# Optimization experiments

Measured on AMD Instinct MI355X. Metric: run time of the kernel, lower is better.

The kernel has to match this reference:

```python
import jax, jax.numpy as jnp
import numpy as np

EPS = 1e-12  # torch F.normalize eps


def _l1_normalize(x, axis):
    denom = jnp.maximum(jnp.sum(jnp.abs(x), axis=axis, keepdims=True), EPS)
    return x / denom


def setup_inputs() -> dict:
    key = jax.random.key(0)
    k1, k2, k3, k4, k5 = jax.random.split(key, 5)
    B, N, M, F_atom, F_bond, F_out = 16, 1024, 12, 128, 32, 128
    stdv = 1.0 / np.sqrt(F_out)
    atom = jax.random.normal(k1, (B, N, F_atom), dtype=jnp.float32)
    bond = jax.random.normal(k2, (B, N, M, F_bond), dtype=jnp.float32)
    adj_matrix = jax.random.randint(k3, (B, N, M), 0, N, dtype=jnp.int64)
    weight_atom_1 = jax.random.uniform(k4, (F_atom, F_out), dtype=jnp.float32, minval=-stdv, maxval=stdv)
    bias_atom_1 = jax.random.uniform(k5, (F_out,), dtype=jnp.float32, minval=-stdv, maxval=stdv)
    return {
        "atom": atom,
        "bond": bond,
        "adj_matrix": adj_matrix,
        "weight_atom_1": weight_atom_1,
        "bias_atom_1": bias_atom_1,
    }


def reference(atom, bond, adj_matrix, weight_atom_1, bias_atom_1):
    # atom: (B,N,F); bond: (B,N,M,Fb); adj_matrix: (B,N,M)
    # Per-batch neighbor gather: atom_neighbor[b,n,m] = atom[b, adj[b,n,m]]
    atom_neighbor = jax.vmap(lambda a, idx: a[idx])(atom, adj_matrix)  # (B,N,M,F)
    atom_neighbor = jnp.mean(atom_neighbor, axis=-2)  # (B,N,F)

    # Bond-norm chain
    bond_norm = jnp.sqrt(jnp.sum(bond * bond, axis=-1))       # (B,N,M) L2 norm
    bond_norm = bond_norm ** (-2.0)                            # inverse square
    bond_norm = _l1_normalize(bond_norm, axis=-1)              # over M
    bond_norm = jnp.prod(bond_norm, axis=2)                    # (B,N)
    bond_norm = _l1_normalize(bond_norm, axis=0)               # over B
    bond_norm = bond_norm ** (-1.0)
    bond_norm = _l1_normalize(bond_norm, axis=1)               # over N

    atom_update = (atom + atom_neighbor) * bond_norm[:, :, None]
    atom_update = jnp.matmul(atom_update, weight_atom_1) + bias_atom_1
    return jax.nn.relu(atom_update)
```

## Files before the change

### kernel.cpp

```cpp
#include <hip/hip_runtime.h>
#include <hip/hip_bf16.h>

#define EPS 1e-12f

typedef __bf16 bf16x8 __attribute__((ext_vector_type(8)));
typedef float  f32x4  __attribute__((ext_vector_type(4)));


__global__ __launch_bounds__(256) void k_bond(const float* __restrict__ bond,
                                              float* __restrict__ p_out) {
    const int gwave = (blockIdx.x * 256 + threadIdx.x) >> 6;
    const int lane  = threadIdx.x & 63;
    const float* base = bond + (size_t)gwave * 384;

    float x[12];
#pragma unroll
    for (int i = 0; i < 6; ++i) {
        float v  = base[lane + 64 * i];
        float sq = v * v;
#pragma unroll
        for (int off = 16; off >= 1; off >>= 1) sq += __shfl_xor(sq, off);
        float s0 = __shfl(sq, 0);
        float s1 = __shfl(sq, 32);
        x[2 * i]     = 1.0f / s0;
        x[2 * i + 1] = 1.0f / s1;
    }
    float sum = 0.f;
#pragma unroll
    for (int m = 0; m < 12; ++m) sum += x[m];
    float d = fmaxf(sum, EPS);
    float prod = 1.f;
#pragma unroll
    for (int m = 0; m < 12; ++m) prod *= x[m] / d;
    if (lane == 0) p_out[gwave] = prod;
}

__global__ __launch_bounds__(256) void k_norm(const float* __restrict__ p,
                                              const float* __restrict__ W,
                                              float* __restrict__ scale,
                                              __bf16* __restrict__ Wt) {
    const int t = threadIdx.x;
    if (blockIdx.x < 16) {
        const int b = blockIdx.x;
        float r[4];
        float partial = 0.f;
#pragma unroll
        for (int i = 0; i < 4; ++i) {
            int n = t + 256 * i;
            float cs = 0.f;
#pragma unroll
            for (int bb = 0; bb < 16; ++bb) cs += p[bb * 1024 + n];
            float y = p[b * 1024 + n] / fmaxf(cs, EPS);
            r[i] = 1.0f / y;
            partial += r[i];
        }
        __shared__ float red[4];
        float v = partial;
#pragma unroll
        for (int off = 32; off >= 1; off >>= 1) v += __shfl_xor(v, off);
        if ((t & 63) == 0) red[t >> 6] = v;
        __syncthreads();
        float S = fmaxf(red[0] + red[1] + red[2] + red[3], EPS);
#pragma unroll
        for (int i = 0; i < 4; ++i) {
            int n = t + 256 * i;
            scale[b * 1024 + n] = r[i] / S;
        }
    } else {
        const int kb = blockIdx.x - 16;
        for (int idx = t; idx < 8 * 128; idx += 256) {
            int k = kb * 8 + (idx >> 7);
            int j = idx & 127;
            Wt[j * 128 + k] = (__bf16)W[k * 128 + j];
        }
    }
}

__global__ __launch_bounds__(256) void k_main(const float* __restrict__ atom,
                                              const int* __restrict__ adj,
                                              const float* __restrict__ scale,
                                              const __bf16* __restrict__ Wt,
                                              const float* __restrict__ bias,
                                              float* __restrict__ out) {
    __shared__ __bf16 uA[32][136];
    __shared__ float  sScale[32];
    __shared__ int    sAdj[32 * 12];

    const int t = threadIdx.x;
    const int rowbase = blockIdx.x * 32;
    const int b = rowbase >> 10;

    if (t < 32) sScale[t] = scale[rowbase + t];
    for (int idx = t; idx < 32 * 12; idx += 256) sAdj[idx] = adj[rowbase * 12 + idx];
    __syncthreads();

    {
        const int j = t & 127;
        const int half = t >> 7;
        const float* atomB = atom + (size_t)b * (1024 * 128);
#pragma unroll 4
        for (int r = half; r < 32; r += 2) {
            float accn = 0.f;
#pragma unroll
            for (int m = 0; m < 12; ++m) {
                int idx = sAdj[r * 12 + m];
                accn += atomB[idx * 128 + j];
            }
            float u = (atom[(size_t)(rowbase + r) * 128 + j] + accn * (1.0f / 12.0f)) * sScale[r];
            uA[r][j] = (__bf16)u;
        }
    }
    __syncthreads();

    const int wave = t >> 6, lane = t & 63;
    const int r0 = (wave >> 1) * 16;
    const int c0 = (wave & 1) * 64;
    const int quad = lane >> 4, lrow = lane & 15;

    bf16x8 aF[4];
#pragma unroll
    for (int kc = 0; kc < 4; ++kc)
        aF[kc] = *(const bf16x8*)&uA[r0 + lrow][kc * 32 + quad * 8];

    f32x4 acc[4];
#pragma unroll
    for (int nt = 0; nt < 4; ++nt) acc[nt] = (f32x4){0.f, 0.f, 0.f, 0.f};

#pragma unroll
    for (int nt = 0; nt < 4; ++nt) {
        const int col = c0 + nt * 16 + lrow;
        const __bf16* wb = Wt + col * 128 + quad * 8;
#pragma unroll
        for (int kc = 0; kc < 4; ++kc) {
            bf16x8 bF = *(const bf16x8*)(wb + kc * 32);
            acc[nt] = __builtin_amdgcn_mfma_f32_16x16x32_bf16(aF[kc], bF, acc[nt], 0, 0, 0);
        }
    }

#pragma unroll
    for (int nt = 0; nt < 4; ++nt) {
        const int col = c0 + nt * 16 + lrow;
        const float bv = bias[col];
#pragma unroll
        for (int i = 0; i < 4; ++i) {
            const int r = r0 + quad * 4 + i;
            float v = acc[nt][i] + bv;
            out[(size_t)(rowbase + r) * 128 + col] = fmaxf(v, 0.f);
        }
    }
}

extern "C" void kernel_launch(void* const* d_in, const int* in_sizes, int n_in,
                              void* d_out, int out_size, void* d_ws, size_t ws_size,
                              hipStream_t stream) {
    const float* atom = (const float*)d_in[0];
    const float* bond = (const float*)d_in[1];
    const int*   adj  = (const int*)d_in[2];
    const float* W    = (const float*)d_in[3];
    const float* bias = (const float*)d_in[4];
    float* out = (float*)d_out;

    char* ws = (char*)d_ws;
    float*  p     = (float*)ws;
    float*  scale = (float*)(ws + 65536);
    __bf16* Wt    = (__bf16*)(ws + 131072);

    hipLaunchKernelGGL(k_bond, dim3(4096), dim3(256), 0, stream, bond, p);
    hipLaunchKernelGGL(k_norm, dim3(32),   dim3(256), 0, stream, p, W, scale, Wt);
    hipLaunchKernelGGL(k_main, dim3(512),  dim3(256), 0, stream, atom, adj, scale, Wt, bias, out);
}
```

Baseline: 110.4 us.

## Fuse norm kernel into bond and main kernels, cutting a launch

The bond-norm reduction now uses 4 threads per row with vectorized float4 loads and shuffle combines, and the weight transpose moves into the same launch. The per-batch normalization that used to run in k_norm is recomputed redundantly inside every k_main block. This removes one kernel launch and one global round trip. In exchange, each main block performs 16K extra reads of p, which should hit in cache. Output stores become nontemporal, and the product is rewritten as prod/d^12, which may underflow differently.

```diff
diff --git a/kernel.cpp b/kernel.cpp
--- a/kernel.cpp
+++ b/kernel.cpp
@@ -8,90 +8,91 @@
 
 
 __global__ __launch_bounds__(256) void k_bond(const float* __restrict__ bond,
-                                              float* __restrict__ p_out) {
-    const int gwave = (blockIdx.x * 256 + threadIdx.x) >> 6;
-    const int lane  = threadIdx.x & 63;
-    const float* base = bond + (size_t)gwave * 384;
-
-    float x[12];
-#pragma unroll
-    for (int i = 0; i < 6; ++i) {
-        float v  = base[lane + 64 * i];
-        float sq = v * v;
-#pragma unroll
-        for (int off = 16; off >= 1; off >>= 1) sq += __shfl_xor(sq, off);
-        float s0 = __shfl(sq, 0);
-        float s1 = __shfl(sq, 32);
-        x[2 * i]     = 1.0f / s0;
-        x[2 * i + 1] = 1.0f / s1;
-    }
-    float sum = 0.f;
-#pragma unroll
-    for (int m = 0; m < 12; ++m) sum += x[m];
-    float d = fmaxf(sum, EPS);
-    float prod = 1.f;
-#pragma unroll
-    for (int m = 0; m < 12; ++m) prod *= x[m] / d;
-    if (lane == 0) p_out[gwave] = prod;
-}
-
-__global__ __launch_bounds__(256) void k_norm(const float* __restrict__ p,
                                               const float* __restrict__ W,
-                                              float* __restrict__ scale,
+                                              float* __restrict__ p_out,
                                               __bf16* __restrict__ Wt) {
     const int t = threadIdx.x;
-    if (blockIdx.x < 16) {
-        const int b = blockIdx.x;
-        float r[4];
-        float partial = 0.f;
+    if (blockIdx.x < 256) {
+        const int gtid = blockIdx.x * 256 + t;
+        const int row  = gtid >> 2;
+        const int q    = gtid & 3;
+        const float* base = bond + (size_t)row * 384 + q * 96;
+
+        float x[3];
 #pragma unroll
-        for (int i = 0; i < 4; ++i) {
-            int n = t + 256 * i;
-            float cs = 0.f;
+        for (int mm = 0; mm < 3; ++mm) {
+            float s = 0.f;
 #pragma unroll
-            for (int bb = 0; bb < 16; ++bb) cs += p[bb * 1024 + n];
-            float y = p[b * 1024 + n] / fmaxf(cs, EPS);
-            r[i] = 1.0f / y;
-            partial += r[i];
+            for (int j = 0; j < 8; ++j) {
+                f32x4 v = *(const f32x4*)(base + mm * 32 + j * 4);
+                s = fmaf(v.x, v.x, s);
+                s = fmaf(v.y, v.y, s);
+                s = fmaf(v.z, v.z, s);
+                s = fmaf(v.w, v.w, s);
+            }
+            x[mm] = 1.0f / s;
         }
-        __shared__ float red[4];
-        float v = partial;
-#pragma unroll
-        for (int off = 32; off >= 1; off >>= 1) v += __shfl_xor(v, off);
-        if ((t & 63) == 0) red[t >> 6] = v;
-        __syncthreads();
-        float S = fmaxf(red[0] + red[1] + red[2] + red[3], EPS);
-#pragma unroll
-        for (int i = 0; i < 4; ++i) {
-            int n = t + 256 * i;
-            scale[b * 1024 + n] = r[i] / S;
+        float sum  = x[0] + x[1] + x[2];
+        float prod = x[0] * x[1] * x[2];
+        sum  += __shfl_xor(sum, 1);  prod *= __shfl_xor(prod, 1);
+        sum  += __shfl_xor(sum, 2);  prod *= __shfl_xor(prod, 2);
+        if (q == 0) {
+            float d   = fmaxf(sum, EPS);
+            float d2  = d * d;
+            float d3  = d2 * d;
+            float d6  = d3 * d3;
+            float d12 = d6 * d6;
+            p_out[row] = prod / d12;
         }
     } else {
-        const int kb = blockIdx.x - 16;
-        for (int idx = t; idx < 8 * 128; idx += 256) {
-            int k = kb * 8 + (idx >> 7);
-            int j = idx & 127;
-            Wt[j * 128 + k] = (__bf16)W[k * 128 + j];
+        const int base = (blockIdx.x - 256) * 4096;
+#pragma unroll
+        for (int i = 0; i < 16; ++i) {
+            int idx = base + t + 256 * i;
+            int k = idx >> 7, j = idx & 127;
+            Wt[j * 128 + k] = (__bf16)W[idx];
         }
     }
 }
 
 __global__ __launch_bounds__(256) void k_main(const float* __restrict__ atom,
                                               const int* __restrict__ adj,
-                                              const float* __restrict__ scale,
+                                              const float* __restrict__ p,
                                               const __bf16* __restrict__ Wt,
                                               const float* __restrict__ bias,
                                               float* __restrict__ out) {
     __shared__ __bf16 uA[32][136];
     __shared__ float  sScale[32];
     __shared__ int    sAdj[32 * 12];
+    __shared__ float  red[4];
 
     const int t = threadIdx.x;
     const int rowbase = blockIdx.x * 32;
     const int b = rowbase >> 10;
 
-    if (t < 32) sScale[t] = scale[rowbase + t];
     for (int idx = t; idx < 32 * 12; idx += 256) sAdj[idx] = adj[rowbase * 12 + idx];
+
+    float S_part = 0.f;
+#pragma unroll
+    for (int i = 0; i < 4; ++i) {
+        int n = t + 256 * i;
+        float cs = 0.f;
+#pragma unroll
+        for (int bb = 0; bb < 16; ++bb) cs += p[bb * 1024 + n];
+        S_part += fmaxf(cs, EPS) / p[b * 1024 + n];
+    }
+#pragma unroll
+    for (int off = 32; off >= 1; off >>= 1) S_part += __shfl_xor(S_part, off);
+    if ((t & 63) == 0) red[t >> 6] = S_part;
+    __syncthreads();
+    const float S = fmaxf(red[0] + red[1] + red[2] + red[3], EPS);
+    if (t < 32) {
+        int nl = (rowbase & 1023) + t;
+        float cs = 0.f;
+#pragma unroll
+        for (int bb = 0; bb < 16; ++bb) cs += p[bb * 1024 + nl];
+        sScale[t] = (fmaxf(cs, EPS) / p[rowbase + t]) / S;
+    }
     __syncthreads();
 
     {
@@ -144,8 +145,8 @@
 #pragma unroll
         for (int i = 0; i < 4; ++i) {
             const int r = r0 + quad * 4 + i;
-            float v = acc[nt][i] + bv;
-            out[(size_t)(rowbase + r) * 128 + col] = fmaxf(v, 0.f);
+            float v = fmaxf(acc[nt][i] + bv, 0.f);
+            __builtin_nontemporal_store(v, &out[(size_t)(rowbase + r) * 128 + col]);
         }
     }
 }
@@ -161,11 +162,9 @@
     float* out = (float*)d_out;
 
     char* ws = (char*)d_ws;
-    float*  p     = (float*)ws;
-    float*  scale = (float*)(ws + 65536);
-    __bf16* Wt    = (__bf16*)(ws + 131072);
+    float*  p  = (float*)ws;
+    __bf16* Wt = (__bf16*)(ws + 65536);
 
-    hipLaunchKernelGGL(k_bond, dim3(4096), dim3(256), 0, stream, bond, p);
-    hipLaunchKernelGGL(k_norm, dim3(32),   dim3(256), 0, stream, p, W, scale, Wt);
-    hipLaunchKernelGGL(k_main, dim3(512),  dim3(256), 0, stream, atom, adj, scale, Wt, bias, out);
+    hipLaunchKernelGGL(k_bond, dim3(260), dim3(256), 0, stream, bond, W, p, Wt);
+    hipLaunchKernelGGL(k_main, dim3(512), dim3(256), 0, stream, atom, adj, p, Wt, bias, out);
 }
```

New measurement: 104.5 us. 1.06x faster.
